# Performance work log

Measured on AMD Instinct MI355X. Metric: run time of the kernel, lower is better.

Reference implementation:

```python
import jax, jax.numpy as jnp
import numpy as np

VOCAB, EMB, HID = 50257, 512, 1024
B, S = 64, 512

def setup_inputs() -> dict:
    key = jax.random.key(0)
    ks = jax.random.split(key, 10)
    sc = lambda fan_in: 1.0 / np.sqrt(fan_in)
    return {
        "x":   jax.random.randint(ks[0], (B, S), 0, VOCAB, dtype=jnp.int32),
        "emb": jax.random.normal(ks[1], (VOCAB, EMB), jnp.float32) * 0.02,
        "Wi1": jax.random.normal(ks[2], (EMB, HID), jnp.float32) * sc(EMB),
        "Wh1": jax.random.normal(ks[3], (HID, HID), jnp.float32) * sc(HID),
        "b1":  jnp.zeros((HID,), jnp.float32),
        "Wi2": jax.random.normal(ks[4], (HID, HID), jnp.float32) * sc(HID),
        "Wh2": jax.random.normal(ks[5], (HID, HID), jnp.float32) * sc(HID),
        "b2":  jnp.zeros((HID,), jnp.float32),
        "Wd":  jax.random.normal(ks[6], (HID, 1), jnp.float32) * sc(HID),
        "bd":  jnp.zeros((1,), jnp.float32),
    }

def reference(x, emb, Wi1, Wh1, b1, Wi2, Wh2, b2, Wd, bd):
    # Embed tokens: [B, S, EMB]
    xe = emb[x]
    batch = x.shape[0]
    hid = Wh1.shape[0]
    h0 = jnp.zeros((batch, hid), xe.dtype)

    # Fused two-layer Elman scan over time. SimpleCell: h' = tanh(x@Wi + b + h@Wh).
    # Dropout is deterministic at inference (train=False) -> identity.
    def step(carry, xt):
        h1, h2 = carry
        h1 = jnp.tanh(xt @ Wi1 + b1 + h1 @ Wh1)
        h2 = jnp.tanh(h1 @ Wi2 + b2 + h2 @ Wh2)
        return (h1, h2), None

    (_, h2_last), _ = jax.lax.scan(step, (h0, h0), jnp.swapaxes(xe, 0, 1))
    logits = h2_last @ Wd + bd  # [B, 1]
    return jax.nn.sigmoid(logits).squeeze(-1)
```

## Files before the change

### kernel.cpp

```cpp
#include <hip/hip_runtime.h>

#define B_   64
#define S_   512
#define EMB_ 512
#define HID_ 1024
#define NBLK_ 256

typedef float    f32x4 __attribute__((ext_vector_type(4)));
typedef unsigned u32x4 __attribute__((ext_vector_type(4)));

__device__ __forceinline__ f32x4 ld_coh4(const float* p) {
    f32x4 d;
    asm volatile("global_load_dwordx4 %0, %1, off sc0 sc1" : "=v"(d) : "v"(p));
    return d;
}
__device__ __forceinline__ void st_coh4(float* p, f32x4 v) {
    asm volatile("global_store_dwordx4 %0, %1, off sc0 sc1" :: "v"(p), "v"(v) : "memory");
}
__device__ __forceinline__ void st_coh1u(unsigned* p, unsigned v) {
    asm volatile("global_store_dword %0, %1, off sc0 sc1" :: "v"(p), "v"(v) : "memory");
}
__device__ __forceinline__ unsigned ld_cohu_wait(const unsigned* p) {
    unsigned d;
    asm volatile("global_load_dword %0, %1, off sc0 sc1\n\t"
                 "s_waitcnt vmcnt(0)"
                 : "=v"(d) : "v"(p) : "memory");
    return d;
}
__device__ __forceinline__ u32x4 ld_coh4u_wait(const unsigned* p) {
    u32x4 d;
    asm volatile("global_load_dwordx4 %0, %1, off sc0 sc1\n\t"
                 "s_waitcnt vmcnt(0)"
                 : "=v"(d) : "v"(p) : "memory");
    return d;
}

__global__ __launch_bounds__(256) void embed_gemm(
    const int* __restrict__ x, const float* __restrict__ emb,
    const float* __restrict__ Wi1, const float* __restrict__ b1,
    float* __restrict__ X1)
{
    __shared__ int   tok[128];
    __shared__ float aT[32][132];
    __shared__ float bl[32][68];

    const int tid = threadIdx.x;
    const int m0  = blockIdx.y * 128;
    const int n0  = blockIdx.x * 64;

    if (tid < 128) {
        int m = m0 + tid;
        tok[tid] = x[(m & 63) * S_ + (m >> 6)];
    }
    __syncthreads();

    const int tx = tid & 15;
    const int ty = tid >> 4;

    float acc[8][4];
#pragma unroll
    for (int r = 0; r < 8; ++r)
#pragma unroll
        for (int c = 0; c < 4; ++c) acc[r][c] = 0.f;

    for (int kt = 0; kt < EMB_; kt += 32) {
#pragma unroll
        for (int j = 0; j < 4; ++j) {
            int idx = tid + j * 256;
            int r   = idx >> 3;
            int k4  = (idx & 7) * 4;
            float4 v = *(const float4*)(emb + (size_t)tok[r] * EMB_ + kt + k4);
            aT[k4 + 0][r] = v.x; aT[k4 + 1][r] = v.y;
            aT[k4 + 2][r] = v.z; aT[k4 + 3][r] = v.w;
        }
#pragma unroll
        for (int j = 0; j < 2; ++j) {
            int idx = tid + j * 256;
            int k   = idx >> 4;
            int c4  = (idx & 15) * 4;
            *(float4*)&bl[k][c4] =
                *(const float4*)(Wi1 + (size_t)(kt + k) * HID_ + n0 + c4);
        }
        __syncthreads();

#pragma unroll 4
        for (int k = 0; k < 32; ++k) {
            float4 a0 = *(const float4*)&aT[k][ty * 8];
            float4 a1 = *(const float4*)&aT[k][ty * 8 + 4];
            float4 bv = *(const float4*)&bl[k][tx * 4];
            float ar[8] = {a0.x, a0.y, a0.z, a0.w, a1.x, a1.y, a1.z, a1.w};
            float bc[4] = {bv.x, bv.y, bv.z, bv.w};
#pragma unroll
            for (int r = 0; r < 8; ++r)
#pragma unroll
                for (int c = 0; c < 4; ++c) acc[r][c] += ar[r] * bc[c];
        }
        __syncthreads();
    }

    float4 bias = *(const float4*)(b1 + n0 + tx * 4);
#pragma unroll
    for (int r = 0; r < 8; ++r) {
        int m = m0 + ty * 8 + r;
        float4 o;
        o.x = acc[r][0] + bias.x; o.y = acc[r][1] + bias.y;
        o.z = acc[r][2] + bias.z; o.w = acc[r][3] + bias.w;
        *(float4*)(X1 + (size_t)m * HID_ + n0 + tx * 4) = o;
    }
}

__device__ __forceinline__ f32x4 shfl_xor4(f32x4 v, int m) {
    f32x4 r;
#pragma unroll
    for (int e = 0; e < 4; ++e) r[e] = __shfl_xor(v[e], m, 64);
    return r;
}

__global__ __launch_bounds__(256, 1) void rnn_scan(
    const float* __restrict__ X1, const float* __restrict__ Wh1,
    const float* __restrict__ Wi2, const float* __restrict__ Wh2,
    const float* __restrict__ b2, float* __restrict__ hb,
    float* __restrict__ pbuf,
    unsigned int* __restrict__ flagsA, unsigned int* __restrict__ flagsB)
{
    __shared__ float w1s[128 * 64];
    __shared__ float w2s[128 * 64];
    __shared__ float w3s[128 * 64];

    const int tid = threadIdx.x;
    const int bk  = blockIdx.x;
    const int rg  = bk >> 7;
    const int kg  = (bk >> 4) & 7;
    const int cg  = bk & 15;
    const int jj  = bk & 127;
    const int k0  = kg * 128;
    const int cs0 = cg * 64;
    const int r0  = rg * 32;

    for (int idx = tid; idx < 2048; idx += 256) {
        int k = idx >> 4, c4 = (idx & 15) * 4;
        *(f32x4*)&w1s[k * 64 + c4] = *(const f32x4*)(Wh1 + (size_t)(k0 + k) * HID_ + cs0 + c4);
        *(f32x4*)&w2s[k * 64 + c4] = *(const f32x4*)(Wi2 + (size_t)(k0 + k) * HID_ + cs0 + c4);
        *(f32x4*)&w3s[k * 64 + c4] = *(const f32x4*)(Wh2 + (size_t)(k0 + k) * HID_ + cs0 + c4);
    }

    const int row32 = tid >> 3;
    const int c8    = tid & 7;
    const int kq8   = tid & 7;

    const f32x4 b2va = *(const f32x4*)(b2 + jj * 8);
    const f32x4 b2vb = *(const f32x4*)(b2 + jj * 8 + 4);

    float* h1buf[2] = { hb, hb + 65536 };
    float* h2buf[2] = { hb + 131072, hb + 196608 };

    __syncthreads();

    for (int i = 0; i <= S_; ++i) {
        if (i >= 1) {
            const unsigned* fb = flagsB + (size_t)(i - 1) * 256 + rg * 128;
            if (tid < 6) {
                const unsigned* fp = (tid < 4) ? (fb + kg * 16 + tid * 4)
                                               : (fb + cg * 8 + (tid - 4) * 4);
                for (;;) {
                    u32x4 v = ld_coh4u_wait(fp);
                    if (v[0] && v[1] && v[2] && v[3]) break;
                    __builtin_amdgcn_s_sleep(1);
                }
            }
            __syncthreads();
        }

        const float* h1src = h1buf[(i + 1) & 1] + (r0 + row32) * HID_ + k0;
        const float* h2src = h2buf[i & 1]       + (r0 + row32) * HID_ + k0;

        f32x4 a1lo = {0,0,0,0}, a1hi = {0,0,0,0};
        f32x4 a2lo = {0,0,0,0}, a2hi = {0,0,0,0};

        f32x4 A1[4], A2[4], B1[4], B2[4];

#pragma unroll
        for (int r = 0; r < 4; ++r) {
            A1[r] = ld_coh4(h1src + r * 4);
            A2[r] = ld_coh4(h2src + r * 4);
        }

#pragma unroll
        for (int it = 0; it < 8; ++it) {
            if (it < 7) {
                const int kn = (it + 1) * 16;
                if (it & 1) {
#pragma unroll
                    for (int r = 0; r < 4; ++r) {
                        A1[r] = ld_coh4(h1src + kn + r * 4);
                        A2[r] = ld_coh4(h2src + kn + r * 4);
                    }
                } else {
#pragma unroll
                    for (int r = 0; r < 4; ++r) {
                        B1[r] = ld_coh4(h1src + kn + r * 4);
                        B2[r] = ld_coh4(h2src + kn + r * 4);
                    }
                }
            }
            if (it < 7) asm volatile("s_waitcnt vmcnt(8)" ::: "memory");
            else        asm volatile("s_waitcnt vmcnt(0)" ::: "memory");
            __builtin_amdgcn_sched_barrier(0);

            const f32x4* c1 = (it & 1) ? B1 : A1;
            const f32x4* c2 = (it & 1) ? B2 : A2;

#pragma unroll
            for (int q = 0; q < 4; ++q) {
#pragma unroll
                for (int e = 0; e < 4; ++e) {
                    const int kk = it * 16 + q * 4 + e;
                    const float hx = c1[q][e];
                    const float hy = c2[q][e];
                    const float* w1r = &w1s[kk * 64 + c8 * 8];
                    const float* w2r = &w2s[kk * 64 + c8 * 8];
                    const float* w3r = &w3s[kk * 64 + c8 * 8];
                    f32x4 wv1a = *(const f32x4*)(w1r);
                    f32x4 wv1b = *(const f32x4*)(w1r + 4);
                    f32x4 wv2a = *(const f32x4*)(w2r);
                    f32x4 wv2b = *(const f32x4*)(w2r + 4);
                    f32x4 wv3a = *(const f32x4*)(w3r);
                    f32x4 wv3b = *(const f32x4*)(w3r + 4);
                    a1lo += hx * wv1a;  a1hi += hx * wv1b;
                    a2lo += hx * wv2a + hy * wv3a;
                    a2hi += hx * wv2b + hy * wv3b;
                }
            }
        }

        {
            float* pp = pbuf + (((size_t)kg * 64 + r0 + row32) * 128
                                + cg * 8 + c8) * 16;
            st_coh4(pp,      a1lo);
            st_coh4(pp + 4,  a1hi);
            st_coh4(pp + 8,  a2lo);
            st_coh4(pp + 12, a2hi);
        }

        asm volatile("s_waitcnt vmcnt(0)" ::: "memory");
        __syncthreads();
        if (tid == 0) st_coh1u(flagsA + (size_t)i * 256 + bk, 1u);

        {
            const unsigned* fa = flagsA + (size_t)i * 256 + rg * 128;
            if (tid < 8) {
                while (ld_cohu_wait(fa + tid * 16 + (jj >> 3)) == 0)
                    __builtin_amdgcn_s_sleep(1);
            }
            __syncthreads();
        }

        {
            const float* qp = pbuf + (((size_t)kq8 * 64 + r0 + row32) * 128
                                      + jj) * 16;
            f32x4 s1a = ld_coh4(qp);
            f32x4 s1b = ld_coh4(qp + 4);
            f32x4 s2a = ld_coh4(qp + 8);
            f32x4 s2b = ld_coh4(qp + 12);

            f32x4 xva = {0,0,0,0}, xvb = {0,0,0,0};
            if (i < S_) {
                const float* xp = X1 + ((size_t)i * B_ + r0 + row32) * HID_ + jj * 8;
                xva = *(const f32x4*)(xp);
                xvb = *(const f32x4*)(xp + 4);
            }

            asm volatile("s_waitcnt vmcnt(0)" ::: "memory");
            __builtin_amdgcn_sched_barrier(0);

#pragma unroll
            for (int m = 1; m <= 4; m <<= 1) {
                s1a += shfl_xor4(s1a, m);
                s1b += shfl_xor4(s1b, m);
                s2a += shfl_xor4(s2a, m);
                s2b += shfl_xor4(s2b, m);
            }

            if (kq8 == 0) {
                const int row = r0 + row32;
                if (i < S_) {
                    f32x4 oa, ob;
#pragma unroll
                    for (int e = 0; e < 4; ++e) {
                        oa[e] = tanhf(xva[e] + s1a[e]);
                        ob[e] = tanhf(xvb[e] + s1b[e]);
                    }
                    float* hp = h1buf[i & 1] + row * HID_ + jj * 8;
                    st_coh4(hp, oa); st_coh4(hp + 4, ob);
                }
                if (i >= 1) {
                    f32x4 oa, ob;
#pragma unroll
                    for (int e = 0; e < 4; ++e) {
                        oa[e] = tanhf(s2a[e] + b2va[e]);
                        ob[e] = tanhf(s2b[e] + b2vb[e]);
                    }
                    float* hp = h2buf[(i + 1) & 1] + row * HID_ + jj * 8;
                    st_coh4(hp, oa); st_coh4(hp + 4, ob);
                }
            }
        }

        if (i < S_) {
            asm volatile("s_waitcnt vmcnt(0)" ::: "memory");
            __syncthreads();
            if (tid == 0) st_coh1u(flagsB + (size_t)i * 256 + bk, 1u);
        }
    }
}

__global__ void dense_sigmoid(const float* __restrict__ h2,
                              const float* __restrict__ Wd,
                              const float* __restrict__ bd,
                              float* __restrict__ out)
{
    int b = blockIdx.x, lane = threadIdx.x;
    float s = 0.f;
    for (int j = lane; j < HID_; j += 64) s += h2[b * HID_ + j] * Wd[j];
#pragma unroll
    for (int off = 32; off > 0; off >>= 1) s += __shfl_down(s, off, 64);
    if (lane == 0) out[b] = 1.f / (1.f + expf(-(s + bd[0])));
}

extern "C" void kernel_launch(void* const* d_in, const int* in_sizes, int n_in,
                              void* d_out, int out_size, void* d_ws, size_t ws_size,
                              hipStream_t stream)
{
    const int*   x   = (const int*)  d_in[0];
    const float* emb = (const float*)d_in[1];
    const float* Wi1 = (const float*)d_in[2];
    const float* Wh1 = (const float*)d_in[3];
    const float* b1  = (const float*)d_in[4];
    const float* Wi2 = (const float*)d_in[5];
    const float* Wh2 = (const float*)d_in[6];
    const float* b2  = (const float*)d_in[7];
    const float* Wd  = (const float*)d_in[8];
    const float* bd  = (const float*)d_in[9];
    float* out = (float*)d_out;

    char* w = (char*)d_ws;
    float*        hb     = (float*)w;
    unsigned int* flagsA = (unsigned int*)(w + 1048576);
    unsigned int* flagsB = (unsigned int*)(w + 1573888);
    float*        pbuf   = (float*)(w + 2098176);
    float*        X1     = (float*)(w + 6292480);

    hipMemsetAsync(w, 0, 2098176, stream);

    dim3 gA(HID_ / 64, (S_ * B_) / 128);
    embed_gemm<<<gA, dim3(256), 0, stream>>>(x, emb, Wi1, b1, X1);

    const float* X1c = X1;
    void* args[] = { (void*)&X1c, (void*)&Wh1, (void*)&Wi2, (void*)&Wh2,
                     (void*)&b2, (void*)&hb, (void*)&pbuf,
                     (void*)&flagsA, (void*)&flagsB };
    hipLaunchCooperativeKernel((const void*)rnn_scan, dim3(NBLK_), dim3(256),
                               args, 0, stream);

    dense_sigmoid<<<64, 64, 0, stream>>>(hb + 196608, Wd, bd, out);
}
```

Before: 12.19 ms.

## Stage hidden-state tiles in LDS and use 4x2 register tiling for recurrent matvec

Each block now loads its 32x128 slices of h1 and h2 from global memory into padded shared-memory tiles. Each thread then computes a 4-row by 2-column register tile, so every weight value read from LDS is reused across four batch rows instead of one. Before, each thread handled one row and 8 columns and streamed h directly from global memory. The partial sums pass through an LDS scratch buffer to restore the original pbuf write layout. This adds two extra __syncthreads per step and about 55 KB more LDS, in exchange for less LDS weight traffic per FMA.

```diff
diff --git a/kernel.cpp b/kernel.cpp
--- a/kernel.cpp
+++ b/kernel.cpp
@@ -7,6 +7,7 @@
 #define NBLK_ 256
 
 typedef float    f32x4 __attribute__((ext_vector_type(4)));
+typedef float    f32x2 __attribute__((ext_vector_type(2)));
 typedef unsigned u32x4 __attribute__((ext_vector_type(4)));
 
 __device__ __forceinline__ f32x4 ld_coh4(const float* p) {
@@ -126,6 +127,9 @@
     __shared__ float w1s[128 * 64];
     __shared__ float w2s[128 * 64];
     __shared__ float w3s[128 * 64];
+    __shared__ float h1s[32 * 132];
+    __shared__ float h2s[32 * 132];
+    __shared__ float scr[256 * 20];
 
     const int tid = threadIdx.x;
     const int bk  = blockIdx.x;
@@ -144,9 +148,10 @@
         *(f32x4*)&w3s[k * 64 + c4] = *(const f32x4*)(Wh2 + (size_t)(k0 + k) * HID_ + cs0 + c4);
     }
 
-    const int row32 = tid >> 3;
-    const int c8    = tid & 7;
-    const int kq8   = tid & 7;
+    const int rq  = tid >> 5;
+    const int cq  = tid & 31;
+    const int oct = cq >> 2;
+    const int pio = (cq & 3) * 2;
 
     const f32x4 b2va = *(const f32x4*)(b2 + jj * 8);
     const f32x4 b2vb = *(const f32x4*)(b2 + jj * 8 + 4);
@@ -171,75 +176,101 @@
             __syncthreads();
         }
 
-        const float* h1src = h1buf[(i + 1) & 1] + (r0 + row32) * HID_ + k0;
-        const float* h2src = h2buf[i & 1]       + (r0 + row32) * HID_ + k0;
-
-        f32x4 a1lo = {0,0,0,0}, a1hi = {0,0,0,0};
-        f32x4 a2lo = {0,0,0,0}, a2hi = {0,0,0,0};
-
-        f32x4 A1[4], A2[4], B1[4], B2[4];
-
-#pragma unroll
-        for (int r = 0; r < 4; ++r) {
-            A1[r] = ld_coh4(h1src + r * 4);
-            A2[r] = ld_coh4(h2src + r * 4);
-        }
-
-#pragma unroll
-        for (int it = 0; it < 8; ++it) {
-            if (it < 7) {
-                const int kn = (it + 1) * 16;
-                if (it & 1) {
-#pragma unroll
-                    for (int r = 0; r < 4; ++r) {
-                        A1[r] = ld_coh4(h1src + kn + r * 4);
-                        A2[r] = ld_coh4(h2src + kn + r * 4);
-                    }
-                } else {
-#pragma unroll
-                    for (int r = 0; r < 4; ++r) {
-                        B1[r] = ld_coh4(h1src + kn + r * 4);
-                        B2[r] = ld_coh4(h2src + kn + r * 4);
-                    }
-                }
-            }
-            if (it < 7) asm volatile("s_waitcnt vmcnt(8)" ::: "memory");
-            else        asm volatile("s_waitcnt vmcnt(0)" ::: "memory");
+        {
+            const float* h1src = h1buf[(i + 1) & 1] + r0 * HID_ + k0;
+            const float* h2src = h2buf[i & 1]       + r0 * HID_ + k0;
+            f32x4 v1[4], v2[4];
+#pragma unroll
+            for (int j = 0; j < 4; ++j) {
+                int u   = tid + j * 256;
+                int row = u >> 5;
+                int kk  = (u & 31) * 4;
+                v1[j] = ld_coh4(h1src + row * HID_ + kk);
+                v2[j] = ld_coh4(h2src + row * HID_ + kk);
+            }
+            asm volatile("s_waitcnt vmcnt(0)" ::: "memory");
             __builtin_amdgcn_sched_barrier(0);
-
-            const f32x4* c1 = (it & 1) ? B1 : A1;
-            const f32x4* c2 = (it & 1) ? B2 : A2;
-
-#pragma unroll
-            for (int q = 0; q < 4; ++q) {
-#pragma unroll
-                for (int e = 0; e < 4; ++e) {
-                    const int kk = it * 16 + q * 4 + e;
-                    const float hx = c1[q][e];
-                    const float hy = c2[q][e];
-                    const float* w1r = &w1s[kk * 64 + c8 * 8];
-                    const float* w2r = &w2s[kk * 64 + c8 * 8];
-                    const float* w3r = &w3s[kk * 64 + c8 * 8];
-                    f32x4 wv1a = *(const f32x4*)(w1r);
-                    f32x4 wv1b = *(const f32x4*)(w1r + 4);
-                    f32x4 wv2a = *(const f32x4*)(w2r);
-                    f32x4 wv2b = *(const f32x4*)(w2r + 4);
-                    f32x4 wv3a = *(const f32x4*)(w3r);
-                    f32x4 wv3b = *(const f32x4*)(w3r + 4);
-                    a1lo += hx * wv1a;  a1hi += hx * wv1b;
-                    a2lo += hx * wv2a + hy * wv3a;
-                    a2hi += hx * wv2b + hy * wv3b;
-                }
-            }
-        }
-
-        {
-            float* pp = pbuf + (((size_t)kg * 64 + r0 + row32) * 128
-                                + cg * 8 + c8) * 16;
-            st_coh4(pp,      a1lo);
-            st_coh4(pp + 4,  a1hi);
-            st_coh4(pp + 8,  a2lo);
-            st_coh4(pp + 12, a2hi);
+#pragma unroll
+            for (int j = 0; j < 4; ++j) {
+                int u   = tid + j * 256;
+                int row = u >> 5;
+                int kk  = (u & 31) * 4;
+                *(f32x4*)&h1s[row * 132 + kk] = v1[j];
+                *(f32x4*)&h2s[row * 132 + kk] = v2[j];
+            }
+            __syncthreads();
+        }
+
+        const float* h1r = &h1s[(rq * 4) * 132];
+        const float* h2r = &h2s[(rq * 4) * 132];
+        const float* wp1 = &w1s[cq * 2];
+        const float* wp2 = &w2s[cq * 2];
+        const float* wp3 = &w3s[cq * 2];
+
+        float a10[2] = {0.f, 0.f}, a11[2] = {0.f, 0.f};
+        float a12[2] = {0.f, 0.f}, a13[2] = {0.f, 0.f};
+        float a20[2] = {0.f, 0.f}, a21[2] = {0.f, 0.f};
+        float a22[2] = {0.f, 0.f}, a23[2] = {0.f, 0.f};
+
+#pragma unroll 4
+        for (int kq = 0; kq < 32; ++kq) {
+            const int kk = kq * 4;
+            f32x4 h1v0 = *(const f32x4*)(h1r + 0 * 132 + kk);
+            f32x4 h1v1 = *(const f32x4*)(h1r + 1 * 132 + kk);
+            f32x4 h1v2 = *(const f32x4*)(h1r + 2 * 132 + kk);
+            f32x4 h1v3 = *(const f32x4*)(h1r + 3 * 132 + kk);
+            f32x4 h2v0 = *(const f32x4*)(h2r + 0 * 132 + kk);
+            f32x4 h2v1 = *(const f32x4*)(h2r + 1 * 132 + kk);
+            f32x4 h2v2 = *(const f32x4*)(h2r + 2 * 132 + kk);
+            f32x4 h2v3 = *(const f32x4*)(h2r + 3 * 132 + kk);
+#pragma unroll
+            for (int j = 0; j < 4; ++j) {
+                const int k = kk + j;
+                f32x2 wa = *(const f32x2*)(wp1 + k * 64);
+                f32x2 wb = *(const f32x2*)(wp2 + k * 64);
+                f32x2 wc = *(const f32x2*)(wp3 + k * 64);
+                a10[0] += h1v0[j] * wa[0];  a10[1] += h1v0[j] * wa[1];
+                a11[0] += h1v1[j] * wa[0];  a11[1] += h1v1[j] * wa[1];
+                a12[0] += h1v2[j] * wa[0];  a12[1] += h1v2[j] * wa[1];
+                a13[0] += h1v3[j] * wa[0];  a13[1] += h1v3[j] * wa[1];
+                a20[0] += h1v0[j] * wb[0] + h2v0[j] * wc[0];
+                a20[1] += h1v0[j] * wb[1] + h2v0[j] * wc[1];
+                a21[0] += h1v1[j] * wb[0] + h2v1[j] * wc[0];
+                a21[1] += h1v1[j] * wb[1] + h2v1[j] * wc[1];
+                a22[0] += h1v2[j] * wb[0] + h2v2[j] * wc[0];
+                a22[1] += h1v2[j] * wb[1] + h2v2[j] * wc[1];
+                a23[0] += h1v3[j] * wb[0] + h2v3[j] * wc[0];
+                a23[1] += h1v3[j] * wb[1] + h2v3[j] * wc[1];
+            }
+        }
+
+        {
+            float* s0 = &scr[((rq * 4 + 0) * 8 + oct) * 20];
+            float* s1 = &scr[((rq * 4 + 1) * 8 + oct) * 20];
+            float* s2 = &scr[((rq * 4 + 2) * 8 + oct) * 20];
+            float* s3 = &scr[((rq * 4 + 3) * 8 + oct) * 20];
+            s0[pio] = a10[0]; s0[pio + 1] = a10[1];
+            s0[8 + pio] = a20[0]; s0[9 + pio] = a20[1];
+            s1[pio] = a11[0]; s1[pio + 1] = a11[1];
+            s1[8 + pio] = a21[0]; s1[9 + pio] = a21[1];
+            s2[pio] = a12[0]; s2[pio + 1] = a12[1];
+            s2[8 + pio] = a22[0]; s2[9 + pio] = a22[1];
+            s3[pio] = a13[0]; s3[pio + 1] = a13[1];
+            s3[8 + pio] = a23[0]; s3[9 + pio] = a23[1];
+        }
+        __syncthreads();
+        {
+            const float* su = &scr[tid * 20];
+            f32x4 u0 = *(const f32x4*)(su);
+            f32x4 u1 = *(const f32x4*)(su + 4);
+            f32x4 u2 = *(const f32x4*)(su + 8);
+            f32x4 u3 = *(const f32x4*)(su + 12);
+            float* pp = pbuf + (((size_t)kg * 64 + r0 + (tid >> 3)) * 128
+                                + cg * 8 + (tid & 7)) * 16;
+            st_coh4(pp,      u0);
+            st_coh4(pp + 4,  u1);
+            st_coh4(pp + 8,  u2);
+            st_coh4(pp + 12, u3);
         }
 
         asm volatile("s_waitcnt vmcnt(0)" ::: "memory");
@@ -256,6 +287,8 @@
         }
 
         {
+            const int row32 = tid >> 3;
+            const int kq8   = tid & 7;
             const float* qp = pbuf + (((size_t)kq8 * 64 + r0 + row32) * 128
                                       + jj) * 16;
             f32x4 s1a = ld_coh4(qp);
```

Measured after the change: 11.67 ms. 4.3% less time.
